# Performance work log

Measured on AMD Instinct MI355X. Metric: run time of the kernel, lower is better.

## Reference

```python
import jax, jax.numpy as jnp
import numpy as np

B, S, F, K = 64, 1024, 128, 64  # batch, seq(=l), feat(=d), bottleneck k


def setup_inputs() -> dict:
    key = jax.random.key(0)
    ks = jax.random.split(key, 24)
    r = lambda k_, sh, s=0.05: (jax.random.normal(k_, sh, dtype=jnp.float32) * s)
    inp = {
        'f1_norm': jax.random.normal(ks[0], (B, S, F), dtype=jnp.float32),
        'f2_norm': jax.random.normal(ks[1], (B, S, F), dtype=jnp.float32),
        'f3_norm': jax.random.normal(ks[2], (B, S, F), dtype=jnp.float32),
        # AMLP params (Linear(F, 2F))
        'Wi': r(ks[3], (2 * F, F)), 'bi': r(ks[4], (2 * F,)),
        'Wq': r(ks[5], (2 * F, F)), 'bq': r(ks[6], (2 * F,)),
        'Wvp': r(ks[7], (2 * F, F)), 'bvp': r(ks[8], (2 * F,)),
        # affine_{a,v,l}: Linear(l, l, bias=False) -> weight [l, l]
        'Aa': r(ks[9], (S, S)), 'Av': r(ks[10], (S, S)), 'Al': r(ks[11], (S, S)),
        # W_{a,v,t}: Linear(l, k) -> [k, l]
        'Wa': r(ks[12], (K, S)), 'Wv': r(ks[13], (K, S)), 'Wt': r(ks[14], (K, S)),
        # W_c{a,v,t}: Linear(2d, k) -> [k, 2F]
        'Wca': r(ks[15], (K, 2 * F)), 'Wcv': r(ks[16], (K, 2 * F)), 'Wct': r(ks[17], (K, 2 * F)),
        # W_h{a,v,t}: Linear(k, l) -> [l, k]
        'Wha': r(ks[18], (S, K)), 'Whv': r(ks[19], (S, K)), 'Wht': r(ks[20], (S, K)),
    }
    return inp


def _amlp(txt, aud, vis, Wi, bi, Wq, bq, Wvp, bvp):
    f1 = jnp.einsum('bsf,gf->bsg', txt, Wi) + bi  # [B,S,2F]
    f2 = jnp.einsum('bsf,gf->bsg', aud, Wq) + bq
    f3 = jnp.einsum('bsf,gf->bsg', vis, Wvp) + bvp
    n1 = jnp.linalg.norm(f1)
    n2 = jnp.linalg.norm(f2)
    n3 = jnp.linalg.norm(f3)
    # faithful to source: third term is scalar factor3 * norm3 (broadcast)
    exp_out = (n1 / (n1 + n2)) * f1 + (n2 / (n1 + n2)) * f2 + (n3 / (n1 + n2 + n3)) * n3
    b, s, g = exp_out.shape
    z = exp_out.reshape(b, s, g // 2, 2).sum(-1)  # AvgPool1d(2,2) * 2 == pair sum
    # F.normalize default dim=1 (over sequence axis for 3D tensor)
    z = z / jnp.maximum(jnp.linalg.norm(z, axis=1, keepdims=True), 1e-12)
    return z  # [B,S,F]


def reference(f1_norm, f2_norm, f3_norm, Wi, bi, Wq, bq, Wvp, bvp,
              Aa, Av, Al, Wa, Wv, Wt, Wca, Wcv, Wct, Wha, Whv, Wht):
    txt, aud, vis = f1_norm, f2_norm, f3_norm
    G = _amlp(txt, aud, vis, Wi, bi, Wq, bq, Wvp, bvp)  # [B,S,F]

    G_ag = jnp.concatenate([aud, G], axis=-1)  # [B,S,2F]
    G_vg = jnp.concatenate([vis, G], axis=-1)
    G_lg = jnp.concatenate([txt, G], axis=-1)
    scale = np.sqrt(G_ag.shape[-1]).astype(np.float32)  # sqrt(2F); same for all three

    # a_j = affine(G_xg^T); att = x^T @ a_j^T  ==  x^T @ (A @ G_xg)
    AGa = jnp.einsum('ts,bsc->btc', Aa, G_ag)
    C_a = jnp.tanh(jnp.einsum('bsf,bsc->bfc', aud, AGa) / scale)  # [B,F,2F]
    AGv = jnp.einsum('ts,bsc->btc', Av, G_ag)  # NOTE: source bug uses G_ag, not G_vg
    C_v = jnp.tanh(jnp.einsum('bsf,bsc->bfc', vis, AGv) / scale)
    AGl = jnp.einsum('ts,bsc->btc', Al, G_lg)
    C_t = jnp.tanh(jnp.einsum('bsf,bsc->bfc', txt, AGl) / scale)

    H_a = jax.nn.relu(jnp.einsum('bfc,kc->bfk', C_a, Wca) + jnp.einsum('bsf,ks->bfk', aud, Wa))
    H_v = jax.nn.relu(jnp.einsum('bfc,kc->bfk', C_v, Wcv) + jnp.einsum('bsf,ks->bfk', vis, Wv))
    H_t = jax.nn.relu(jnp.einsum('bfc,kc->bfk', C_t, Wct) + jnp.einsum('bsf,ks->bfk', txt, Wt))

    out_a = jnp.einsum('bfk,sk->bsf', H_a, Wha) + aud  # [B,S,F]
    out_v = jnp.einsum('bfk,sk->bsf', H_v, Whv) + vis
    out_t = jnp.einsum('bfk,sk->bsf', H_t, Wht) + txt
    return (out_t, out_a, out_v)
```

## Files before the change

kernel.cpp:

```cpp
#include <hip/hip_runtime.h>
#include <math.h>

constexpr int Bb = 64;
constexpr int Ss = 1024;
constexpr int Ff = 128;
constexpr int G2 = 256;
constexpr int Kk = 64;
constexpr int NE = 1152;

typedef __bf16 bfrag __attribute__((ext_vector_type(8)));
typedef float  facc  __attribute__((ext_vector_type(4)));
typedef short  s8v   __attribute__((ext_vector_type(8)));

__device__ __forceinline__ short f2bfs(float f) {
  union { float f; unsigned u; } v; v.f = f;
  unsigned r = v.u + 0x7FFFu + ((v.u >> 16) & 1u);
  return (short)(r >> 16);
}
__device__ __forceinline__ float bf2fs(short s) {
  union { unsigned u; float f; } v; v.u = ((unsigned)(unsigned short)s) << 16;
  return v.f;
}
__device__ __forceinline__ facc mfma16(bfrag a, bfrag b, facc c) {
  return __builtin_amdgcn_mfma_f32_16x16x32_bf16(a, b, c, 0, 0, 0);
}

__global__ void k_transpose(const float* __restrict__ aud, const float* __restrict__ vis,
                            const float* __restrict__ txt, short* __restrict__ xT) {
  __shared__ float tile[64][65];
  int z = blockIdx.z;
  int mod = z >> 6, b = z & 63;
  const float* x = (mod == 0) ? aud : (mod == 1) ? vis : txt;
  int s0 = blockIdx.x * 64, f0 = blockIdx.y * 64;
  int tid = threadIdx.x;
  for (int i = 0; i < 16; ++i) {
    int idx = i * 256 + tid;
    int si = idx >> 6, fi = idx & 63;
    tile[si][fi] = x[((size_t)b * Ss + s0 + si) * Ff + f0 + fi];
  }
  __syncthreads();
  short* dst = xT + ((size_t)mod * Bb + b) * Ff * Ss;
  for (int i = 0; i < 16; ++i) {
    int idx = i * 256 + tid;
    int fi = idx >> 6, si = idx & 63;
    dst[(size_t)(f0 + fi) * Ss + s0 + si] = f2bfs(tile[si][fi]);
  }
}

__global__ void k_build_aextT(const float* __restrict__ Aa, const float* __restrict__ Av,
                              const float* __restrict__ Al, const float* __restrict__ Wa,
                              const float* __restrict__ Wv, const float* __restrict__ Wt,
                              short* __restrict__ aextT) {
  __shared__ float tile[64][65];
  int mod = blockIdx.z;
  const float* A = (mod == 0) ? Aa : (mod == 1) ? Av : Al;
  const float* W = (mod == 0) ? Wa : (mod == 1) ? Wv : Wt;
  short* dst = aextT + (size_t)mod * NE * Ss;
  int n0 = blockIdx.x * 64, t0 = blockIdx.y * 64;
  int tid = threadIdx.x;
  if (n0 < Ss) {
    for (int i = 0; i < 16; ++i) {
      int idx = i * 256 + tid;
      int ti = idx >> 6, nj = idx & 63;
      tile[ti][nj] = A[(size_t)(t0 + ti) * Ss + n0 + nj];
    }
    __syncthreads();
    for (int i = 0; i < 16; ++i) {
      int idx = i * 256 + tid;
      int nj = idx >> 6, ti = idx & 63;
      dst[(size_t)(n0 + nj) * Ss + t0 + ti] = f2bfs(tile[ti][nj]);
    }
  } else if (n0 < Ss + Kk) {
    for (int i = 0; i < 16; ++i) {
      int idx = i * 256 + tid;
      int j = idx >> 6, tt = idx & 63;
      dst[(size_t)(n0 + j) * Ss + t0 + tt] = f2bfs(W[(size_t)(n0 - Ss + j) * Ss + t0 + tt]);
    }
  } else {
    for (int i = 0; i < 16; ++i) {
      int idx = i * 256 + tid;
      int j = idx >> 6, tt = idx & 63;
      dst[(size_t)(n0 + j) * Ss + t0 + tt] = 0;
    }
  }
}

__global__ void k_build_w(const float* __restrict__ Wca, const float* __restrict__ Wcv,
                          const float* __restrict__ Wct, const float* __restrict__ Wha,
                          const float* __restrict__ Whv, const float* __restrict__ Wht,
                          const float* __restrict__ Wi, const float* __restrict__ Wq,
                          const float* __restrict__ Wvp,
                          short* __restrict__ wcb, short* __restrict__ whb,
                          short* __restrict__ wbar) {
  int idx = blockIdx.x * 256 + threadIdx.x;
  const int n1 = 3 * Kk * G2;
  const int n2 = n1 + 3 * Ss * Kk;
  if (idx < n1) {
    int mod = idx / (Kk * G2), r = idx - mod * (Kk * G2);
    const float* W = (mod == 0) ? Wca : (mod == 1) ? Wcv : Wct;
    wcb[idx] = f2bfs(W[r]);
  } else if (idx < n2) {
    int j = idx - n1;
    int mod = j / (Ss * Kk), r = j - mod * (Ss * Kk);
    const float* W = (mod == 0) ? Wha : (mod == 1) ? Whv : Wht;
    whb[j] = f2bfs(W[r]);
  } else {
    int j = idx - n2;
    int mod = j / (G2 * Ff), r = j - mod * (G2 * Ff);
    int n = r >> 7, k = r & 127;
    const float* W = (mod == 0) ? Wi : (mod == 1) ? Wq : Wvp;
    wbar[mod * G2 * Ff + (((k >> 3) * G2 + n) * 8) + (k & 7)] = f2bfs(W[r]);
  }
}

__global__ void __launch_bounds__(256) k_amlp(
    const float* __restrict__ txt, const float* __restrict__ aud, const float* __restrict__ vis,
    const float* __restrict__ bi, const float* __restrict__ bq, const float* __restrict__ bvp,
    const short* __restrict__ wbar,
    short* __restrict__ p1, short* __restrict__ p2, float* __restrict__ sumsq) {
  int mod = blockIdx.y;
  const float* x    = (mod == 0) ? txt : (mod == 1) ? aud : vis;
  const float* bias = (mod == 0) ? bi  : (mod == 1) ? bq  : bvp;
  const short* wbm  = wbar + mod * G2 * Ff;
  short* pout = (mod == 0) ? p1 : (mod == 1) ? p2 : nullptr;

  __shared__ short wlds[G2 * Ff];
  __shared__ float wred[4];
  int tid = threadIdx.x, lane = tid & 63, wave = tid >> 6;
  int quad = lane >> 4, nl = lane & 15;
  for (int i = 0; i < 16; ++i) {
    int o = (i * 256 + tid) * 8;
    *(s8v*)(wlds + o) = *(const s8v*)(wbm + o);
  }
  __syncthreads();

  int arow = blockIdx.x * 64 + wave * 16 + nl;
  const float* xrow = x + (size_t)arow * Ff;
  facc zero = {0.f, 0.f, 0.f, 0.f};
  facc acc[16];
  for (int t = 0; t < 16; ++t) acc[t] = zero;
  for (int k0 = 0; k0 < Ff; k0 += 32) {
    float4 a0 = *(const float4*)(xrow + k0 + quad * 8);
    float4 a1 = *(const float4*)(xrow + k0 + quad * 8 + 4);
    bfrag af;
    af[0]=(__bf16)a0.x; af[1]=(__bf16)a0.y; af[2]=(__bf16)a0.z; af[3]=(__bf16)a0.w;
    af[4]=(__bf16)a1.x; af[5]=(__bf16)a1.y; af[6]=(__bf16)a1.z; af[7]=(__bf16)a1.w;
    int chunk = (k0 >> 3) + quad;
    for (int t = 0; t < 16; ++t) {
      bfrag bfr = *(const bfrag*)(wlds + ((size_t)chunk * G2 + t * 16 + nl) * 8);
      acc[t] = mfma16(af, bfr, acc[t]);
    }
  }

  float sq = 0.f;
  int drow = blockIdx.x * 64 + wave * 16 + quad * 4;
  for (int t = 0; t < 16; ++t) {
    float bia = bias[t * 16 + nl];
    for (int r = 0; r < 4; ++r) {
      float fv = acc[t][r] + bia;
      sq += fv * fv;
      if (pout) {
        float fo = fv + __shfl_xor(fv, 1, 64);
        if ((lane & 1) == 0)
          pout[(size_t)(drow + r) * Ff + t * 8 + (nl >> 1)] = f2bfs(fo);
      }
    }
  }
  for (int off = 32; off > 0; off >>= 1) sq += __shfl_down(sq, off, 64);
  if (lane == 0) wred[wave] = sq;
  __syncthreads();
  if (tid == 0) atomicAdd(&sumsq[mod], wred[0] + wred[1] + wred[2] + wred[3]);
}

__global__ void k_colnorm(const short* __restrict__ p1, const short* __restrict__ p2,
                          const float* __restrict__ sumsq, float* __restrict__ colnsq) {
  float n1 = sqrtf(sumsq[0]), n2 = sqrtf(sumsq[1]), n3 = sqrtf(sumsq[2]);
  float w1 = n1 / (n1 + n2), w2 = n2 / (n1 + n2);
  float tc = 2.f * n3 * n3 / (n1 + n2 + n3);
  int b = blockIdx.x, j = threadIdx.x;
  int s0 = blockIdx.y * 64;
  float a = 0.f;
  for (int s = s0; s < s0 + 64; ++s) {
    size_t off = ((size_t)b * Ss + s) * Ff + j;
    float z = w1 * bf2fs(p1[off]) + w2 * bf2fs(p2[off]) + tc;
    a += z * z;
  }
  atomicAdd(&colnsq[b * Ff + j], a);
}

__global__ void k_gnormT(const short* __restrict__ p1, const short* __restrict__ p2,
                         const float* __restrict__ sumsq, const float* __restrict__ colnsq,
                         short* __restrict__ gT) {
  __shared__ float tile[64][65];
  float n1 = sqrtf(sumsq[0]), n2 = sqrtf(sumsq[1]), n3 = sqrtf(sumsq[2]);
  float w1 = n1 / (n1 + n2), w2 = n2 / (n1 + n2);
  float tc = 2.f * n3 * n3 / (n1 + n2 + n3);
  int b = blockIdx.z, s0 = blockIdx.x * 64, f0 = blockIdx.y * 64;
  int tid = threadIdx.x;
  for (int i = 0; i < 16; ++i) {
    int idx = i * 256 + tid;
    int si = idx >> 6, fi = idx & 63;
    size_t off = ((size_t)b * Ss + s0 + si) * Ff + f0 + fi;
    float z = w1 * bf2fs(p1[off]) + w2 * bf2fs(p2[off]) + tc;
    float cn = fmaxf(sqrtf(colnsq[b * Ff + f0 + fi]), 1e-12f);
    tile[si][fi] = z / cn;
  }
  __syncthreads();
  short* dst = gT + (size_t)b * Ff * Ss;
  for (int i = 0; i < 16; ++i) {
    int idx = i * 256 + tid;
    int fi = idx >> 6, si = idx & 63;
    dst[(size_t)(f0 + fi) * Ss + s0 + si] = f2bfs(tile[si][fi]);
  }
}

__global__ void __launch_bounds__(256) k_mgemm(const short* __restrict__ xT,
                                               const short* __restrict__ aextT,
                                               short* __restrict__ mxext) {
  int mod = blockIdx.z;
  const short* Ap = xT + (size_t)mod * Bb * Ff * Ss;
  const short* Bp = aextT + (size_t)mod * NE * Ss;
  short* Op = mxext + (size_t)mod * Bb * Ff * NE;
  int M0 = blockIdx.x * 128, N0 = blockIdx.y * 128;
  __shared__ short As[128 * 32];
  __shared__ short Bs[128 * 32];
  int tid = threadIdx.x, lane = tid & 63, wave = tid >> 6;
  int quad = lane >> 4, nl = lane & 15;
  int wm = (wave >> 1) * 64, wn = (wave & 1) * 64;
  int r0 = tid >> 2, c8 = (tid & 3) * 8;
  facc zero = {0.f, 0.f, 0.f, 0.f};
  facc acc[4][4];
  for (int i = 0; i < 4; ++i) for (int j = 0; j < 4; ++j) acc[i][j] = zero;
  for (int k0 = 0; k0 < Ss; k0 += 32) {
    __syncthreads();
    *(s8v*)(As + tid * 8)        = *(const s8v*)(Ap + (size_t)(M0 + r0) * Ss + k0 + c8);
    *(s8v*)(As + 2048 + tid * 8) = *(const s8v*)(Ap + (size_t)(M0 + 64 + r0) * Ss + k0 + c8);
    *(s8v*)(Bs + tid * 8)        = *(const s8v*)(Bp + (size_t)(N0 + r0) * Ss + k0 + c8);
    *(s8v*)(Bs + 2048 + tid * 8) = *(const s8v*)(Bp + (size_t)(N0 + 64 + r0) * Ss + k0 + c8);
    __syncthreads();
    bfrag a[4], bfr[4];
    for (int mt = 0; mt < 4; ++mt)
      a[mt] = *(const bfrag*)(As + (wm + mt * 16 + nl) * 32 + quad * 8);
    for (int nt = 0; nt < 4; ++nt)
      bfr[nt] = *(const bfrag*)(Bs + (wn + nt * 16 + nl) * 32 + quad * 8);
    for (int mt = 0; mt < 4; ++mt)
      for (int nt = 0; nt < 4; ++nt)
        acc[mt][nt] = mfma16(a[mt], bfr[nt], acc[mt][nt]);
  }
  for (int mt = 0; mt < 4; ++mt)
    for (int nt = 0; nt < 4; ++nt)
      for (int r = 0; r < 4; ++r) {
        int row = M0 + wm + mt * 16 + quad * 4 + r;
        int col = N0 + wn + nt * 16 + nl;
        Op[(size_t)row * NE + col] = f2bfs(acc[mt][nt][r]);
      }
}

__global__ void __launch_bounds__(256) k_cgemm(const short* __restrict__ mxext,
                                               const short* __restrict__ xT,
                                               const short* __restrict__ gT,
                                               short* __restrict__ cc) {
  int b = blockIdx.x, half = blockIdx.y, mod = blockIdx.z;
  const short* Ap = mxext + ((size_t)mod * Bb + b) * Ff * NE;
  const short* Bsrc = (half == 0)
      ? (xT + (size_t)((mod == 2) ? 2 : 0) * Bb * Ff * Ss + (size_t)b * Ff * Ss)
      : (gT + (size_t)b * Ff * Ss);
  short* Cp = cc + ((size_t)mod * Bb + b) * Ff * G2;
  __shared__ short As[128 * 32];
  __shared__ short Bs[128 * 32];
  int tid = threadIdx.x, lane = tid & 63, wave = tid >> 6;
  int quad = lane >> 4, nl = lane & 15;
  int wm = (wave >> 1) * 64, wn = (wave & 1) * 64;
  int r0 = tid >> 2, c8 = (tid & 3) * 8;
  facc zero = {0.f, 0.f, 0.f, 0.f};
  facc acc[4][4];
  for (int i = 0; i < 4; ++i) for (int j = 0; j < 4; ++j) acc[i][j] = zero;
  for (int k0 = 0; k0 < Ss; k0 += 32) {
    __syncthreads();
    *(s8v*)(As + tid * 8)        = *(const s8v*)(Ap + (size_t)r0 * NE + k0 + c8);
    *(s8v*)(As + 2048 + tid * 8) = *(const s8v*)(Ap + (size_t)(64 + r0) * NE + k0 + c8);
    *(s8v*)(Bs + tid * 8)        = *(const s8v*)(Bsrc + (size_t)r0 * Ss + k0 + c8);
    *(s8v*)(Bs + 2048 + tid * 8) = *(const s8v*)(Bsrc + (size_t)(64 + r0) * Ss + k0 + c8);
    __syncthreads();
    bfrag a[4], bfr[4];
    for (int mt = 0; mt < 4; ++mt)
      a[mt] = *(const bfrag*)(As + (wm + mt * 16 + nl) * 32 + quad * 8);
    for (int nt = 0; nt < 4; ++nt)
      bfr[nt] = *(const bfrag*)(Bs + (wn + nt * 16 + nl) * 32 + quad * 8);
    for (int mt = 0; mt < 4; ++mt)
      for (int nt = 0; nt < 4; ++nt)
        acc[mt][nt] = mfma16(a[mt], bfr[nt], acc[mt][nt]);
  }
  for (int mt = 0; mt < 4; ++mt)
    for (int nt = 0; nt < 4; ++nt)
      for (int r = 0; r < 4; ++r) {
        int row = wm + mt * 16 + quad * 4 + r;
        int col = half * 128 + wn + nt * 16 + nl;
        Cp[(size_t)row * G2 + col] = f2bfs(tanhf(acc[mt][nt][r] * 0.0625f));
      }
}

__global__ void k_hgemm(const short* __restrict__ cc, const short* __restrict__ wcb,
                        const short* __restrict__ mxext, short* __restrict__ h) {
  int b = blockIdx.x, mod = blockIdx.y;
  const short* Cp = cc + ((size_t)mod * Bb + b) * Ff * G2;
  const short* Wp = wcb + (size_t)mod * Kk * G2;
  const short* T2 = mxext + ((size_t)mod * Bb + b) * Ff * NE + Ss;
  short* Hp = h + ((size_t)mod * Bb + b) * Ff * Kk;
  int tid = threadIdx.x, lane = tid & 63, wave = tid >> 6;
  int quad = lane >> 4, nl = lane & 15;
  facc zero = {0.f, 0.f, 0.f, 0.f};
  facc acc[2][4];
  for (int i = 0; i < 2; ++i) for (int j = 0; j < 4; ++j) acc[i][j] = zero;
  for (int k0 = 0; k0 < G2; k0 += 32) {
    bfrag a[2], bfr[4];
    for (int mt = 0; mt < 2; ++mt)
      a[mt] = *(const bfrag*)(Cp + (size_t)(wave * 32 + mt * 16 + nl) * G2 + k0 + quad * 8);
    for (int nt = 0; nt < 4; ++nt)
      bfr[nt] = *(const bfrag*)(Wp + (size_t)(nt * 16 + nl) * G2 + k0 + quad * 8);
    for (int mt = 0; mt < 2; ++mt)
      for (int nt = 0; nt < 4; ++nt)
        acc[mt][nt] = mfma16(a[mt], bfr[nt], acc[mt][nt]);
  }
  for (int mt = 0; mt < 2; ++mt)
    for (int nt = 0; nt < 4; ++nt)
      for (int r = 0; r < 4; ++r) {
        int row = wave * 32 + mt * 16 + quad * 4 + r;
        int col = nt * 16 + nl;
        float v = acc[mt][nt][r] + bf2fs(T2[(size_t)row * NE + col]);
        Hp[(size_t)row * Kk + col] = f2bfs(fmaxf(v, 0.f));
      }
}

__global__ void k_outgemm(const short* __restrict__ whb, const short* __restrict__ h,
                          const float* __restrict__ txt, const float* __restrict__ aud,
                          const float* __restrict__ vis, float* __restrict__ outp) {
  int s0 = blockIdx.x * 128, b = blockIdx.y, mod = blockIdx.z;
  const short* Wp = whb + (size_t)mod * Ss * Kk;
  const short* Hp = h + ((size_t)mod * Bb + b) * Ff * Kk;
  const float* xres = ((mod == 0) ? aud : (mod == 1) ? vis : txt) + (size_t)b * Ss * Ff;
  int slot = (mod == 0) ? 1 : (mod == 1) ? 2 : 0;
  float* Op = outp + ((size_t)slot * Bb + b) * Ss * Ff;
  int tid = threadIdx.x, lane = tid & 63, wave = tid >> 6;
  int quad = lane >> 4, nl = lane & 15;
  int wm = (wave >> 1) * 64, wn = (wave & 1) * 64;
  facc zero = {0.f, 0.f, 0.f, 0.f};
  facc acc[4][4];
  for (int i = 0; i < 4; ++i) for (int j = 0; j < 4; ++j) acc[i][j] = zero;
  for (int k0 = 0; k0 < Kk; k0 += 32) {
    bfrag a[4], bfr[4];
    for (int mt = 0; mt < 4; ++mt)
      a[mt] = *(const bfrag*)(Wp + (size_t)(s0 + wm + mt * 16 + nl) * Kk + k0 + quad * 8);
    for (int nt = 0; nt < 4; ++nt)
      bfr[nt] = *(const bfrag*)(Hp + (size_t)(wn + nt * 16 + nl) * Kk + k0 + quad * 8);
    for (int mt = 0; mt < 4; ++mt)
      for (int nt = 0; nt < 4; ++nt)
        acc[mt][nt] = mfma16(a[mt], bfr[nt], acc[mt][nt]);
  }
  for (int mt = 0; mt < 4; ++mt)
    for (int nt = 0; nt < 4; ++nt)
      for (int r = 0; r < 4; ++r) {
        int srow = s0 + wm + mt * 16 + quad * 4 + r;
        int col = wn + nt * 16 + nl;
        size_t o = (size_t)srow * Ff + col;
        Op[o] = acc[mt][nt][r] + xres[o];
      }
}

extern "C" void kernel_launch(void* const* d_in, const int* in_sizes, int n_in,
                              void* d_out, int out_size, void* d_ws, size_t ws_size,
                              hipStream_t stream) {
  const float* txt = (const float*)d_in[0];
  const float* aud = (const float*)d_in[1];
  const float* vis = (const float*)d_in[2];
  const float* Wi  = (const float*)d_in[3];
  const float* bi  = (const float*)d_in[4];
  const float* Wq  = (const float*)d_in[5];
  const float* bq  = (const float*)d_in[6];
  const float* Wvp = (const float*)d_in[7];
  const float* bvp = (const float*)d_in[8];
  const float* Aa  = (const float*)d_in[9];
  const float* Av  = (const float*)d_in[10];
  const float* Al  = (const float*)d_in[11];
  const float* Wa  = (const float*)d_in[12];
  const float* Wv  = (const float*)d_in[13];
  const float* Wt  = (const float*)d_in[14];
  const float* Wca = (const float*)d_in[15];
  const float* Wcv = (const float*)d_in[16];
  const float* Wct = (const float*)d_in[17];
  const float* Wha = (const float*)d_in[18];
  const float* Whv = (const float*)d_in[19];
  const float* Wht = (const float*)d_in[20];

  char* w = (char*)d_ws;
  float* sumsq  = (float*)w;
  float* colnsq = (float*)(w + 256);
  size_t off = 65536;
  short* xT    = (short*)(w + off); off += (size_t)3 * Bb * Ff * Ss * 2;
  short* aextT = (short*)(w + off); off += (size_t)3 * NE * Ss * 2;
  short* gT    = (short*)(w + off); off += (size_t)Bb * Ff * Ss * 2;
  short* mx    = (short*)(w + off);
  short* p1    = mx;
  short* p2    = mx + (size_t)Bb * Ss * Ff;
  off += (size_t)3 * Bb * Ff * NE * 2;
  short* cc    = (short*)(w + off); off += (size_t)3 * Bb * Ff * G2 * 2;
  short* h     = (short*)(w + off); off += (size_t)3 * Bb * Ff * Kk * 2;
  short* wcb   = (short*)(w + off); off += (size_t)3 * Kk * G2 * 2;
  short* whb   = (short*)(w + off); off += (size_t)3 * Ss * Kk * 2;
  short* wbar  = (short*)(w + off); off += (size_t)3 * G2 * Ff * 2;

  hipMemsetAsync(d_ws, 0, 65536, stream);
  k_transpose<<<dim3(16, 2, 192), 256, 0, stream>>>(aud, vis, txt, xT);
  k_build_aextT<<<dim3(NE / 64, 16, 3), 256, 0, stream>>>(Aa, Av, Al, Wa, Wv, Wt, aextT);
  k_build_w<<<(3 * Kk * G2 + 3 * Ss * Kk + 3 * G2 * Ff) / 256, 256, 0, stream>>>(
      Wca, Wcv, Wct, Wha, Whv, Wht, Wi, Wq, Wvp, wcb, whb, wbar);
  k_amlp<<<dim3(Bb * Ss / 64, 3), 256, 0, stream>>>(txt, aud, vis, bi, bq, bvp,
                                                    wbar, p1, p2, sumsq);
  k_colnorm<<<dim3(Bb, 16), 128, 0, stream>>>(p1, p2, sumsq, colnsq);
  k_gnormT<<<dim3(16, 2, Bb), 256, 0, stream>>>(p1, p2, sumsq, colnsq, gT);
  k_mgemm<<<dim3(Bb * Ff / 128, NE / 128, 3), 256, 0, stream>>>(xT, aextT, mx);
  k_cgemm<<<dim3(Bb, 2, 3), 256, 0, stream>>>(mx, xT, gT, cc);
  k_hgemm<<<dim3(Bb, 3), 256, 0, stream>>>(cc, wcb, mx, h);
  k_outgemm<<<dim3(Ss / 128, Bb, 3), 256, 0, stream>>>(whb, h, txt, aud, vis, (float*)d_out);
}
```

Before: 482.8 us.

## Use direct global-to-LDS loads, amortize AMLP weight staging, split cgemm columns

Replaces register-staged global-to-LDS copies in k_amlp, k_mgemm and k_cgemm with the global_load_lds builtin, so tiles go straight to shared memory without passing through VGPRs. k_amlp now handles four 64-row groups per block, so the 64KB weight tile is staged once per 256 rows instead of once per 64, with bias values hoisted into registers. k_cgemm splits its N dimension into four 64-wide tiles, doubling the grid from 384 to 768 blocks to fill more CUs. The cost is fewer amlp blocks (768) with more serial work each, and the A tile in cgemm is re-read by twice as many blocks.

```diff
diff --git a/kernel.cpp b/kernel.cpp
--- a/kernel.cpp
+++ b/kernel.cpp
@@ -23,6 +23,11 @@
 }
 __device__ __forceinline__ facc mfma16(bfrag a, bfrag b, facc c) {
   return __builtin_amdgcn_mfma_f32_16x16x32_bf16(a, b, c, 0, 0, 0);
+}
+__device__ __forceinline__ void gld16(const void* g, void* l) {
+  __builtin_amdgcn_global_load_lds(
+      (const __attribute__((address_space(1))) void*)g,
+      (__attribute__((address_space(3))) void*)l, 16, 0, 0);
 }
 
 __global__ void k_transpose(const float* __restrict__ aud, const float* __restrict__ vis,
@@ -130,39 +135,42 @@
   int quad = lane >> 4, nl = lane & 15;
   for (int i = 0; i < 16; ++i) {
     int o = (i * 256 + tid) * 8;
-    *(s8v*)(wlds + o) = *(const s8v*)(wbm + o);
+    gld16(wbm + o, wlds + o);
   }
   __syncthreads();
 
-  int arow = blockIdx.x * 64 + wave * 16 + nl;
-  const float* xrow = x + (size_t)arow * Ff;
+  float bia[16];
+  for (int t = 0; t < 16; ++t) bia[t] = bias[t * 16 + nl];
+
   facc zero = {0.f, 0.f, 0.f, 0.f};
-  facc acc[16];
-  for (int t = 0; t < 16; ++t) acc[t] = zero;
-  for (int k0 = 0; k0 < Ff; k0 += 32) {
-    float4 a0 = *(const float4*)(xrow + k0 + quad * 8);
-    float4 a1 = *(const float4*)(xrow + k0 + quad * 8 + 4);
-    bfrag af;
-    af[0]=(__bf16)a0.x; af[1]=(__bf16)a0.y; af[2]=(__bf16)a0.z; af[3]=(__bf16)a0.w;
-    af[4]=(__bf16)a1.x; af[5]=(__bf16)a1.y; af[6]=(__bf16)a1.z; af[7]=(__bf16)a1.w;
-    int chunk = (k0 >> 3) + quad;
+  float sq = 0.f;
+  for (int rg = 0; rg < 4; ++rg) {
+    int arow = blockIdx.x * 256 + rg * 64 + wave * 16 + nl;
+    const float* xrow = x + (size_t)arow * Ff;
+    facc acc[16];
+    for (int t = 0; t < 16; ++t) acc[t] = zero;
+    for (int k0 = 0; k0 < Ff; k0 += 32) {
+      float4 a0 = *(const float4*)(xrow + k0 + quad * 8);
+      float4 a1 = *(const float4*)(xrow + k0 + quad * 8 + 4);
+      bfrag af;
+      af[0]=(__bf16)a0.x; af[1]=(__bf16)a0.y; af[2]=(__bf16)a0.z; af[3]=(__bf16)a0.w;
+      af[4]=(__bf16)a1.x; af[5]=(__bf16)a1.y; af[6]=(__bf16)a1.z; af[7]=(__bf16)a1.w;
+      int chunk = (k0 >> 3) + quad;
+      for (int t = 0; t < 16; ++t) {
+        bfrag bfr = *(const bfrag*)(wlds + ((size_t)chunk * G2 + t * 16 + nl) * 8);
+        acc[t] = mfma16(af, bfr, acc[t]);
+      }
+    }
+    int drow = blockIdx.x * 256 + rg * 64 + wave * 16 + quad * 4;
     for (int t = 0; t < 16; ++t) {
-      bfrag bfr = *(const bfrag*)(wlds + ((size_t)chunk * G2 + t * 16 + nl) * 8);
-      acc[t] = mfma16(af, bfr, acc[t]);
-    }
-  }
-
-  float sq = 0.f;
-  int drow = blockIdx.x * 64 + wave * 16 + quad * 4;
-  for (int t = 0; t < 16; ++t) {
-    float bia = bias[t * 16 + nl];
-    for (int r = 0; r < 4; ++r) {
-      float fv = acc[t][r] + bia;
-      sq += fv * fv;
-      if (pout) {
-        float fo = fv + __shfl_xor(fv, 1, 64);
-        if ((lane & 1) == 0)
-          pout[(size_t)(drow + r) * Ff + t * 8 + (nl >> 1)] = f2bfs(fo);
+      for (int r = 0; r < 4; ++r) {
+        float fv = acc[t][r] + bia[t];
+        sq += fv * fv;
+        if (pout) {
+          float fo = fv + __shfl_xor(fv, 1, 64);
+          if ((lane & 1) == 0)
+            pout[(size_t)(drow + r) * Ff + t * 8 + (nl >> 1)] = f2bfs(fo);
+        }
       }
     }
   }
@@ -233,10 +241,10 @@
   for (int i = 0; i < 4; ++i) for (int j = 0; j < 4; ++j) acc[i][j] = zero;
   for (int k0 = 0; k0 < Ss; k0 += 32) {
     __syncthreads();
-    *(s8v*)(As + tid * 8)        = *(const s8v*)(Ap + (size_t)(M0 + r0) * Ss + k0 + c8);
-    *(s8v*)(As + 2048 + tid * 8) = *(const s8v*)(Ap + (size_t)(M0 + 64 + r0) * Ss + k0 + c8);
-    *(s8v*)(Bs + tid * 8)        = *(const s8v*)(Bp + (size_t)(N0 + r0) * Ss + k0 + c8);
-    *(s8v*)(Bs + 2048 + tid * 8) = *(const s8v*)(Bp + (size_t)(N0 + 64 + r0) * Ss + k0 + c8);
+    gld16(Ap + (size_t)(M0 + r0) * Ss + k0 + c8,      As + tid * 8);
+    gld16(Ap + (size_t)(M0 + 64 + r0) * Ss + k0 + c8, As + 2048 + tid * 8);
+    gld16(Bp + (size_t)(N0 + r0) * Ss + k0 + c8,      Bs + tid * 8);
+    gld16(Bp + (size_t)(N0 + 64 + r0) * Ss + k0 + c8, Bs + 2048 + tid * 8);
     __syncthreads();
     bfrag a[4], bfr[4];
     for (int mt = 0; mt < 4; ++mt)
@@ -260,42 +268,43 @@
                                                const short* __restrict__ xT,
                                                const short* __restrict__ gT,
                                                short* __restrict__ cc) {
-  int b = blockIdx.x, half = blockIdx.y, mod = blockIdx.z;
+  int b = blockIdx.x, nt4 = blockIdx.y, mod = blockIdx.z;
   const short* Ap = mxext + ((size_t)mod * Bb + b) * Ff * NE;
-  const short* Bsrc = (half == 0)
-      ? (xT + (size_t)((mod == 2) ? 2 : 0) * Bb * Ff * Ss + (size_t)b * Ff * Ss)
-      : (gT + (size_t)b * Ff * Ss);
+  const short* Bsrc = (nt4 < 2)
+      ? (xT + (size_t)((mod == 2) ? 2 : 0) * Bb * Ff * Ss + (size_t)b * Ff * Ss
+             + (size_t)(nt4 & 1) * 64 * Ss)
+      : (gT + (size_t)b * Ff * Ss + (size_t)(nt4 & 1) * 64 * Ss);
   short* Cp = cc + ((size_t)mod * Bb + b) * Ff * G2;
+  int ncol0 = nt4 * 64;
   __shared__ short As[128 * 32];
-  __shared__ short Bs[128 * 32];
+  __shared__ short Bs[64 * 32];
   int tid = threadIdx.x, lane = tid & 63, wave = tid >> 6;
   int quad = lane >> 4, nl = lane & 15;
-  int wm = (wave >> 1) * 64, wn = (wave & 1) * 64;
+  int wm = (wave >> 1) * 64, wn = (wave & 1) * 32;
   int r0 = tid >> 2, c8 = (tid & 3) * 8;
   facc zero = {0.f, 0.f, 0.f, 0.f};
-  facc acc[4][4];
-  for (int i = 0; i < 4; ++i) for (int j = 0; j < 4; ++j) acc[i][j] = zero;
+  facc acc[4][2];
+  for (int i = 0; i < 4; ++i) for (int j = 0; j < 2; ++j) acc[i][j] = zero;
   for (int k0 = 0; k0 < Ss; k0 += 32) {
     __syncthreads();
-    *(s8v*)(As + tid * 8)        = *(const s8v*)(Ap + (size_t)r0 * NE + k0 + c8);
-    *(s8v*)(As + 2048 + tid * 8) = *(const s8v*)(Ap + (size_t)(64 + r0) * NE + k0 + c8);
-    *(s8v*)(Bs + tid * 8)        = *(const s8v*)(Bsrc + (size_t)r0 * Ss + k0 + c8);
-    *(s8v*)(Bs + 2048 + tid * 8) = *(const s8v*)(Bsrc + (size_t)(64 + r0) * Ss + k0 + c8);
+    gld16(Ap + (size_t)r0 * NE + k0 + c8,        As + tid * 8);
+    gld16(Ap + (size_t)(64 + r0) * NE + k0 + c8, As + 2048 + tid * 8);
+    gld16(Bsrc + (size_t)r0 * Ss + k0 + c8,      Bs + tid * 8);
     __syncthreads();
-    bfrag a[4], bfr[4];
+    bfrag a[4], bfr[2];
     for (int mt = 0; mt < 4; ++mt)
       a[mt] = *(const bfrag*)(As + (wm + mt * 16 + nl) * 32 + quad * 8);
-    for (int nt = 0; nt < 4; ++nt)
+    for (int nt = 0; nt < 2; ++nt)
       bfr[nt] = *(const bfrag*)(Bs + (wn + nt * 16 + nl) * 32 + quad * 8);
     for (int mt = 0; mt < 4; ++mt)
-      for (int nt = 0; nt < 4; ++nt)
+      for (int nt = 0; nt < 2; ++nt)
         acc[mt][nt] = mfma16(a[mt], bfr[nt], acc[mt][nt]);
   }
   for (int mt = 0; mt < 4; ++mt)
-    for (int nt = 0; nt < 4; ++nt)
+    for (int nt = 0; nt < 2; ++nt)
       for (int r = 0; r < 4; ++r) {
         int row = wm + mt * 16 + quad * 4 + r;
-        int col = half * 128 + wn + nt * 16 + nl;
+        int col = ncol0 + wn + nt * 16 + nl;
         Cp[(size_t)row * G2 + col] = f2bfs(tanhf(acc[mt][nt][r] * 0.0625f));
       }
 }
@@ -414,12 +423,12 @@
   k_build_aextT<<<dim3(NE / 64, 16, 3), 256, 0, stream>>>(Aa, Av, Al, Wa, Wv, Wt, aextT);
   k_build_w<<<(3 * Kk * G2 + 3 * Ss * Kk + 3 * G2 * Ff) / 256, 256, 0, stream>>>(
       Wca, Wcv, Wct, Wha, Whv, Wht, Wi, Wq, Wvp, wcb, whb, wbar);
-  k_amlp<<<dim3(Bb * Ss / 64, 3), 256, 0, stream>>>(txt, aud, vis, bi, bq, bvp,
-                                                    wbar, p1, p2, sumsq);
+  k_amlp<<<dim3(Bb * Ss / 256, 3), 256, 0, stream>>>(txt, aud, vis, bi, bq, bvp,
+                                                     wbar, p1, p2, sumsq);
   k_colnorm<<<dim3(Bb, 16), 128, 0, stream>>>(p1, p2, sumsq, colnsq);
   k_gnormT<<<dim3(16, 2, Bb), 256, 0, stream>>>(p1, p2, sumsq, colnsq, gT);
   k_mgemm<<<dim3(Bb * Ff / 128, NE / 128, 3), 256, 0, stream>>>(xT, aextT, mx);
-  k_cgemm<<<dim3(Bb, 2, 3), 256, 0, stream>>>(mx, xT, gT, cc);
+  k_cgemm<<<dim3(Bb, 4, 3), 256, 0, stream>>>(mx, xT, gT, cc);
   k_hgemm<<<dim3(Bb, 3), 256, 0, stream>>>(cc, wcb, mx, h);
   k_outgemm<<<dim3(Ss / 128, Bb, 3), 256, 0, stream>>>(whb, h, txt, aud, vis, (float*)d_out);
 }
```

New measurement: 478.2 us. Within noise of the previous version (-1.0%).
